# Kernel optimization log

Hardware: AMD Instinct MI355X
Metric: run time of the kernel (lower is better)

Reference implementation:

```python
import jax, jax.numpy as jnp
import numpy as np

HIDDEN = 384
HEADS = 8
DIM_HEAD = HIDDEN // HEADS  # 48
INNER = DIM_HEAD * HEADS
SCALE = DIM_HEAD ** -0.5


def setup_inputs() -> dict:
    key = jax.random.key(0)
    k1, k2, k3, k4 = jax.random.split(key, 4)
    B, C, D, H, W = 2, HIDDEN, 16, 16, 8
    x = jax.random.normal(k1, (B, C, D, H, W), dtype=jnp.float32)
    # nn.Linear weights (stored as [out, in] in torch; use [in, out] here)
    w_qkv = jax.random.normal(k2, (C, 3 * INNER), dtype=jnp.float32) * (C ** -0.5)
    w_out = jax.random.normal(k3, (INNER, C), dtype=jnp.float32) * (INNER ** -0.5)
    b_out = jax.random.normal(k4, (C,), dtype=jnp.float32) * 0.02
    return {"x": x, "w_qkv": w_qkv, "w_out": w_out, "b_out": b_out}


def reference(x, w_qkv, w_out, b_out):
    B, C, D, H, W = x.shape
    N = D * H * W
    tokens = x.reshape(B, C, N).transpose(0, 2, 1)          # [B, N, C]
    qkv = tokens @ w_qkv                                     # [B, N, 3*inner]
    qkv = qkv.reshape(B, N, 3, HEADS, DIM_HEAD).transpose(2, 0, 3, 1, 4)
    q, k, v = qkv[0], qkv[1], qkv[2]                         # [B, h, N, dh]
    q = jnp.clip(q, -5.0, 5.0)
    k = jnp.clip(k, -5.0, 5.0)
    logits = jnp.einsum('bhnd,bhmd->bhnm', q, k) * SCALE     # [B, h, N, N]
    logits = logits - jnp.max(logits, axis=-1, keepdims=True)
    attn = jax.nn.softmax(logits, axis=-1)
    out = jnp.einsum('bhnm,bhmd->bhnd', attn, v)             # [B, h, N, dh]
    out = out.transpose(0, 2, 1, 3).reshape(B, N, INNER)     # [B, N, inner]
    out = out @ w_out + b_out                                # [B, N, C]
    out = out.transpose(0, 2, 1).reshape(B, C, D, H, W)
    return x + out
```

## Files before the change

kernel.cpp:

```cpp
#include <hip/hip_runtime.h>

#define B_SZ 2
#define C_IN 384
#define N_TOK 2048
#define HEADS 8
#define DH 48
#define J3 1152
#define QSCALE_LOG2 0.20823509110768f
#define KSPLIT 4
#define KEYS_PER_SPLIT 512
#define DEFER_THR 11.0f

typedef __attribute__((ext_vector_type(8))) _Float16 f16x8;
typedef __attribute__((ext_vector_type(4))) _Float16 f16x4;
typedef __attribute__((ext_vector_type(4))) float f32x4;

__device__ __forceinline__ unsigned short f2h(float f) {
  _Float16 h = (_Float16)f;
  return __builtin_bit_cast(unsigned short, h);
}
__device__ __forceinline__ uint pk2(float a, float b) {
  return __builtin_bit_cast(uint, __builtin_amdgcn_cvt_pkrtz(a, b));
}
__device__ __forceinline__ float exp2g(float x) {
  return __builtin_amdgcn_exp2f(x);
}

__global__ __launch_bounds__(256) void qkv_mfma(
    const float* __restrict__ x, const float* __restrict__ wq,
    unsigned short* __restrict__ Qo, unsigned short* __restrict__ Ko,
    unsigned short* __restrict__ Vo) {
  __shared__ __align__(16) unsigned short Ts[128][72];
  __shared__ __align__(16) unsigned short Ws[64][72];
  __shared__ __align__(16) unsigned short Xt[64][132];
  __shared__ __align__(16) unsigned short Wt[64][68];
  const int tid = threadIdx.x;
  const int w = tid >> 6, lane = tid & 63;
  const int lc = lane & 15, lg = lane >> 4;
  const int m0 = blockIdx.x * 128;
  const int j0 = blockIdx.y * 64;
  const int b = m0 >> 11;
  const int n0 = m0 & 2047;

  f32x4 acc[2][4];
#pragma unroll
  for (int i = 0; i < 2; ++i)
#pragma unroll
    for (int j = 0; j < 4; ++j) acc[i][j] = (f32x4){0.f, 0.f, 0.f, 0.f};

  const float* xbase = x + (size_t)b * C_IN * N_TOK + n0;

  for (int kk = 0; kk < C_IN; kk += 64) {
#pragma unroll
    for (int i = 0; i < 8; ++i) {
      const int f = tid + 256 * i;
      const int c = f >> 5, m4 = (f & 31) * 4;
      const float4 v = *(const float4*)(xbase + (size_t)(kk + c) * N_TOK + m4);
      ushort4 h;
      h.x = f2h(v.x); h.y = f2h(v.y); h.z = f2h(v.z); h.w = f2h(v.w);
      *(ushort4*)&Xt[c][m4] = h;
    }
#pragma unroll
    for (int i = 0; i < 4; ++i) {
      const int f = tid + 256 * i;
      const int c = f >> 4, j4 = (f & 15) * 4;
      const float4 v = *(const float4*)(wq + (size_t)(kk + c) * J3 + j0 + j4);
      ushort4 h;
      h.x = f2h(v.x); h.y = f2h(v.y); h.z = f2h(v.z); h.w = f2h(v.w);
      *(ushort4*)&Wt[c][j4] = h;
    }
    __syncthreads();

    {
      const int m = tid >> 1, ks = (tid & 1) * 32;
      unsigned short tmp[32];
#pragma unroll
      for (int j2 = 0; j2 < 32; ++j2) tmp[j2] = Xt[ks + j2][m];
#pragma unroll
      for (int j2 = 0; j2 < 8; ++j2)
        *(ushort4*)&Ts[m][ks + 4 * j2] =
            make_ushort4(tmp[4 * j2], tmp[4 * j2 + 1], tmp[4 * j2 + 2], tmp[4 * j2 + 3]);
      const int jj = tid >> 2, ks2 = (tid & 3) * 16;
      unsigned short tw[16];
#pragma unroll
      for (int i2 = 0; i2 < 16; ++i2) tw[i2] = Wt[ks2 + i2][jj];
#pragma unroll
      for (int i2 = 0; i2 < 4; ++i2)
        *(ushort4*)&Ws[jj][ks2 + 4 * i2] =
            make_ushort4(tw[4 * i2], tw[4 * i2 + 1], tw[4 * i2 + 2], tw[4 * i2 + 3]);
    }
    __syncthreads();

    f16x8 a[2][2], bf[4][2];
#pragma unroll
    for (int mt = 0; mt < 2; ++mt)
#pragma unroll
      for (int kh = 0; kh < 2; ++kh)
        a[mt][kh] = *(const f16x8*)&Ts[32 * w + 16 * mt + lc][32 * kh + 8 * lg];
#pragma unroll
    for (int jt = 0; jt < 4; ++jt)
#pragma unroll
      for (int kh = 0; kh < 2; ++kh)
        bf[jt][kh] = *(const f16x8*)&Ws[16 * jt + lc][32 * kh + 8 * lg];
#pragma unroll
    for (int mt = 0; mt < 2; ++mt)
#pragma unroll
      for (int jt = 0; jt < 4; ++jt)
#pragma unroll
        for (int kh = 0; kh < 2; ++kh)
          acc[mt][jt] = __builtin_amdgcn_mfma_f32_16x16x32_f16(a[mt][kh], bf[jt][kh], acc[mt][jt], 0, 0, 0);
    __syncthreads();
  }

  if (j0 >= 768) {
    unsigned short* Tv = &Ts[0][0];
#pragma unroll
    for (int jt = 0; jt < 4; ++jt)
#pragma unroll
      for (int mt = 0; mt < 2; ++mt)
#pragma unroll
        for (int r = 0; r < 4; ++r)
          Tv[(16 * jt + lc) * 136 + (32 * w + 16 * mt + 4 * lg + r)] =
              f2h(acc[mt][jt][r]);
    __syncthreads();
#pragma unroll
    for (int i = 0; i < 4; ++i) {
      const int s = tid + i * 256;
      const int row = s >> 4;
      const int segoff = (s & 15) * 8;
      const int rr2 = j0 - 768 + row;
      const int head = rr2 / DH;
      const int d = rr2 - head * DH;
      const int bh = b * HEADS + head;
      *(uint4*)(Vo + ((size_t)bh * DH + d) * N_TOK + n0 + segoff) =
          *(const uint4*)&Tv[row * 136 + segoff];
    }
  } else {
#pragma unroll
    for (int jt = 0; jt < 4; ++jt) {
      const int jlo = j0 + 16 * jt;
      const int which = jlo / 384;
      const int rr = jlo - which * 384;
      const int head = rr / DH;
      const int dbase = rr - head * DH;
      const int d = dbase + lc;
      const int bh = b * HEADS + head;
#pragma unroll
      for (int mt = 0; mt < 2; ++mt)
#pragma unroll
        for (int r = 0; r < 4; ++r) {
          const int n = (m0 + 32 * w + 16 * mt + 4 * lg + r) & 2047;
          float val = fminf(fmaxf(acc[mt][jt][r], -5.f), 5.f);
          if (which == 0) {
            Qo[((size_t)bh * N_TOK + n) * DH + d] = f2h(val * QSCALE_LOG2);
          } else {
            Ko[((size_t)bh * N_TOK + n) * DH + d] = f2h(val);
          }
        }
    }
  }
}

__global__ __launch_bounds__(512) void attn_kernel(
    const unsigned short* __restrict__ Q, const unsigned short* __restrict__ K,
    const unsigned short* __restrict__ Vt, unsigned short* __restrict__ Opart,
    float2* __restrict__ ml) {
  const int qt = blockIdx.x, bh = blockIdx.y, ks = blockIdx.z;
  const int b = bh >> 3, h = bh & 7;
  const int n0 = qt * 128;
  const int tid = threadIdx.x;
  const int w = tid >> 6, lane = tid & 63;
  const int lc = lane & 15, lg = lane >> 4;

  __shared__ __align__(16) unsigned short Ks[2][64][56];
  __shared__ __align__(16) unsigned short Vs[2][48][68];

  const unsigned short* Qrow = Q + ((size_t)bh * N_TOK + n0 + 16 * w + lc) * DH;
  const f16x8 qf0 = *(const f16x8*)(Qrow + 8 * lg);
  f16x8 qf1 = {0, 0, 0, 0, 0, 0, 0, 0};
  {
    const f16x4 t = *(const f16x4*)(Qrow + 32 + 4 * lg);
    qf1[0] = t[0]; qf1[1] = t[1]; qf1[2] = t[2]; qf1[3] = t[3];
  }

  const unsigned short* Kg = K + (size_t)bh * N_TOK * DH + (size_t)ks * KEYS_PER_SPLIT * DH;
  const uint* Vg32 = (const uint*)(Vt + (size_t)bh * DH * N_TOK) + ks * (KEYS_PER_SPLIT / 2);

  uint kr[3], vr[3];
  auto issue = [&](int t0) {
    const uint* Ksrc = (const uint*)(Kg + (size_t)t0 * DH);
#pragma unroll
    for (int i = 0; i < 3; ++i) {
      const int dw = tid + i * 512;
      kr[i] = Ksrc[dw];
      vr[i] = Vg32[(size_t)(dw >> 5) * 1024 + (t0 >> 1) + (dw & 31)];
    }
  };
  auto commit = [&](int buf) {
#pragma unroll
    for (int i = 0; i < 3; ++i) {
      const int dw = tid + i * 512;
      const int key = dw / 24, c = dw - key * 24;
      *(uint*)&Ks[buf][key][2 * c] = kr[i];
      *(uint*)&Vs[buf][dw >> 5][2 * (dw & 31)] = vr[i];
    }
  };

  float m_run = -1e30f, l_run = 0.f;
  f32x4 oacc[3] = {{0,0,0,0},{0,0,0,0},{0,0,0,0}};

  issue(0);
  commit(0);

  for (int t = 0; t < KEYS_PER_SPLIT / 64; ++t) {
    const int cur = t & 1;
    if (t < KEYS_PER_SPLIT / 64 - 1) issue((t + 1) * 64);
    __syncthreads();

    f32x4 sac[4];
    __builtin_amdgcn_s_setprio(1);
#pragma unroll
    for (int it = 0; it < 4; ++it) {
      const int krow = 16 * it + lc;
      const f16x8 kf0 = *(const f16x8*)&Ks[cur][krow][8 * lg];
      f16x8 kf1 = {0, 0, 0, 0, 0, 0, 0, 0};
      const f16x4 tt = *(const f16x4*)&Ks[cur][krow][32 + 4 * lg];
      kf1[0] = tt[0]; kf1[1] = tt[1]; kf1[2] = tt[2]; kf1[3] = tt[3];
      const f32x4 z = {0.f, 0.f, 0.f, 0.f};
      f32x4 s = __builtin_amdgcn_mfma_f32_16x16x32_f16(kf0, qf0, z, 0, 0, 0);
      sac[it]  = __builtin_amdgcn_mfma_f32_16x16x32_f16(kf1, qf1, s, 0, 0, 0);
    }
    __builtin_amdgcn_s_setprio(0);

    float mt = -1e30f;
#pragma unroll
    for (int it = 0; it < 4; ++it)
#pragma unroll
      for (int r = 0; r < 4; ++r) mt = fmaxf(mt, sac[it][r]);
    mt = fmaxf(mt, __shfl_xor(mt, 16, 64));
    mt = fmaxf(mt, __shfl_xor(mt, 32, 64));

    if (!__all(mt - m_run <= DEFER_THR)) {
      const float mn = fmaxf(m_run, mt);
      const float rs = exp2g(m_run - mn);
      m_run = mn;
      l_run *= rs;
#pragma unroll
      for (int itd = 0; itd < 3; ++itd)
#pragma unroll
        for (int r = 0; r < 4; ++r) oacc[itd][r] *= rs;
    }

    float p[4][4];
    float ps = 0.f;
#pragma unroll
    for (int it = 0; it < 4; ++it)
#pragma unroll
      for (int r = 0; r < 4; ++r) {
        p[it][r] = exp2g(sac[it][r] - m_run);
        ps += p[it][r];
      }
    ps += __shfl_xor(ps, 16, 64);
    ps += __shfl_xor(ps, 32, 64);
    l_run += ps;

    f16x8 pt[2];
#pragma unroll
    for (int ks2 = 0; ks2 < 2; ++ks2) {
      union { f16x8 v; uint u[4]; } pu;
      pu.u[0] = pk2(p[2 * ks2][0], p[2 * ks2][1]);
      pu.u[1] = pk2(p[2 * ks2][2], p[2 * ks2][3]);
      pu.u[2] = pk2(p[2 * ks2 + 1][0], p[2 * ks2 + 1][1]);
      pu.u[3] = pk2(p[2 * ks2 + 1][2], p[2 * ks2 + 1][3]);
      pt[ks2] = pu.v;
    }

    __builtin_amdgcn_s_setprio(1);
#pragma unroll
    for (int itd = 0; itd < 3; ++itd) {
      const int drow = 16 * itd + lc;
#pragma unroll
      for (int ks2 = 0; ks2 < 2; ++ks2) {
        const f16x4 v0 = *(const f16x4*)&Vs[cur][drow][4 * lg + 32 * ks2];
        const f16x4 v1 = *(const f16x4*)&Vs[cur][drow][4 * lg + 32 * ks2 + 16];
        f16x8 vf;
        vf[0] = v0[0]; vf[1] = v0[1]; vf[2] = v0[2]; vf[3] = v0[3];
        vf[4] = v1[0]; vf[5] = v1[1]; vf[6] = v1[2]; vf[7] = v1[3];
        oacc[itd] = __builtin_amdgcn_mfma_f32_16x16x32_f16(vf, pt[ks2], oacc[itd], 0, 0, 0);
      }
    }
    __builtin_amdgcn_s_setprio(0);

    if (t < KEYS_PER_SPLIT / 64 - 1) commit(cur ^ 1);
  }

  if (lg == 0)
    ml[(size_t)(ks * 16 + bh) * N_TOK + n0 + 16 * w + lc] = make_float2(m_run, l_run);
  const float inv = 1.f / l_run;
  unsigned short* Ap = Opart +
      ((size_t)(ks * B_SZ + b) * N_TOK + n0 + 16 * w + lc) * 384 + h * DH;
#pragma unroll
  for (int itd = 0; itd < 3; ++itd) {
    uint2 pkv;
    pkv.x = pk2(oacc[itd][0] * inv, oacc[itd][1] * inv);
    pkv.y = pk2(oacc[itd][2] * inv, oacc[itd][3] * inv);
    *(uint2*)(Ap + 16 * itd + 4 * lg) = pkv;
  }
}

__global__ __launch_bounds__(256) void combine_kernel(
    const unsigned short* __restrict__ Opart, const float2* __restrict__ ml,
    unsigned short* __restrict__ AOh) {
  const int vid = blockIdx.x * 256 + threadIdx.x;
  const int c8 = vid % 48;
  const int n  = (vid / 48) & 2047;
  const int b  = vid / (48 * 2048);
  const int c0 = c8 * 8;
  const int h  = c0 / 48;
  const int bh = b * 8 + h;
  const size_t PS = (size_t)B_SZ * N_TOK * 384;
  float2 e0 = ml[(size_t)(0 * 16 + bh) * N_TOK + n];
  float2 e1 = ml[(size_t)(1 * 16 + bh) * N_TOK + n];
  float2 e2 = ml[(size_t)(2 * 16 + bh) * N_TOK + n];
  float2 e3 = ml[(size_t)(3 * 16 + bh) * N_TOK + n];
  const float M = fmaxf(fmaxf(e0.x, e1.x), fmaxf(e2.x, e3.x));
  const float g0 = exp2g(e0.x - M) * e0.y, g1 = exp2g(e1.x - M) * e1.y;
  const float g2 = exp2g(e2.x - M) * e2.y, g3 = exp2g(e3.x - M) * e3.y;
  const float inv = 1.f / (g0 + g1 + g2 + g3);
  const float s0 = g0 * inv, s1 = g1 * inv, s2 = g2 * inv, s3 = g3 * inv;
  const size_t o = ((size_t)b * N_TOK + n) * 384 + c0;
  union U8 { uint4 q; _Float16 e[8]; } u0, u1, u2, u3, r;
  u0.q = *(const uint4*)(Opart + 0 * PS + o);
  u1.q = *(const uint4*)(Opart + 1 * PS + o);
  u2.q = *(const uint4*)(Opart + 2 * PS + o);
  u3.q = *(const uint4*)(Opart + 3 * PS + o);
#pragma unroll
  for (int k = 0; k < 8; k += 2) {
    const float a = (float)u0.e[k] * s0 + (float)u1.e[k] * s1 +
                    (float)u2.e[k] * s2 + (float)u3.e[k] * s3;
    const float bb = (float)u0.e[k + 1] * s0 + (float)u1.e[k + 1] * s1 +
                     (float)u2.e[k + 1] * s2 + (float)u3.e[k + 1] * s3;
    *(uint*)&r.e[k] = pk2(a, bb);
  }
  *(uint4*)(AOh + o) = r.q;
}

__global__ __launch_bounds__(256) void proj_mfma(
    const unsigned short* __restrict__ AOh, const float* __restrict__ wo,
    const float* __restrict__ b_out, const float* __restrict__ x,
    float* __restrict__ out) {
  __shared__ __align__(16) unsigned short As[64][72];
  __shared__ __align__(16) unsigned short Bs[128][72];
  __shared__ __align__(16) unsigned short Wt2[64][68];
  const int tid = threadIdx.x;
  const int w = tid >> 6, lane = tid & 63;
  const int lc = lane & 15, lg = lane >> 4;
  const int c0 = blockIdx.x * 64;
  const int m0 = blockIdx.y * 128;
  const int b = m0 >> 11;

  f32x4 acc[4][2];
#pragma unroll
  for (int i = 0; i < 4; ++i)
#pragma unroll
    for (int j = 0; j < 2; ++j) acc[i][j] = (f32x4){0.f, 0.f, 0.f, 0.f};

  const int brow = tid & 127, bseg = tid >> 7;

  for (int kk = 0; kk < C_IN; kk += 64) {
#pragma unroll
    for (int i = 0; i < 4; ++i) {
      const int f = tid + 256 * i;
      const int c = f >> 4, c4 = (f & 15) * 4;
      const float4 v = *(const float4*)(wo + (size_t)(kk + c) * C_IN + c0 + c4);
      ushort4 h;
      h.x = f2h(v.x); h.y = f2h(v.y); h.z = f2h(v.z); h.w = f2h(v.w);
      *(ushort4*)&Wt2[c][c4] = h;
    }
    {
      const uint4* s2 = (const uint4*)(AOh + (size_t)(m0 + brow) * C_IN + kk + bseg * 32);
      uint4* d2 = (uint4*)&Bs[brow][bseg * 32];
      d2[0] = s2[0]; d2[1] = s2[1]; d2[2] = s2[2]; d2[3] = s2[3];
    }
    __syncthreads();

    {
      const int cc = tid >> 2, ks2 = (tid & 3) * 16;
      unsigned short tw[16];
#pragma unroll
      for (int i2 = 0; i2 < 16; ++i2) tw[i2] = Wt2[ks2 + i2][cc];
#pragma unroll
      for (int i2 = 0; i2 < 4; ++i2)
        *(ushort4*)&As[cc][ks2 + 4 * i2] =
            make_ushort4(tw[4 * i2], tw[4 * i2 + 1], tw[4 * i2 + 2], tw[4 * i2 + 3]);
    }
    __syncthreads();

    f16x8 a[4][2], bf[2][2];
#pragma unroll
    for (int ct = 0; ct < 4; ++ct)
#pragma unroll
      for (int kh = 0; kh < 2; ++kh)
        a[ct][kh] = *(const f16x8*)&As[16 * ct + lc][32 * kh + 8 * lg];
#pragma unroll
    for (int mt = 0; mt < 2; ++mt)
#pragma unroll
      for (int kh = 0; kh < 2; ++kh)
        bf[mt][kh] = *(const f16x8*)&Bs[32 * w + 16 * mt + lc][32 * kh + 8 * lg];
#pragma unroll
    for (int ct = 0; ct < 4; ++ct)
#pragma unroll
      for (int mt = 0; mt < 2; ++mt)
#pragma unroll
        for (int kh = 0; kh < 2; ++kh)
          acc[ct][mt] = __builtin_amdgcn_mfma_f32_16x16x32_f16(a[ct][kh], bf[mt][kh], acc[ct][mt], 0, 0, 0);
    __syncthreads();
  }

#pragma unroll
  for (int ct = 0; ct < 4; ++ct)
#pragma unroll
    for (int r = 0; r < 4; ++r) {
      const int c = c0 + 16 * ct + 4 * lg + r;
      const float bias = b_out[c];
#pragma unroll
      for (int mt = 0; mt < 2; ++mt) {
        const int n = (m0 + 32 * w + 16 * mt + lc) & 2047;
        const size_t off = ((size_t)b * C_IN + c) * N_TOK + n;
        out[off] = x[off] + bias + acc[ct][mt][r];
      }
    }
}

extern "C" void kernel_launch(void* const* d_in, const int* in_sizes, int n_in,
                              void* d_out, int out_size, void* d_ws, size_t ws_size,
                              hipStream_t stream) {
  const float* x     = (const float*)d_in[0];
  const float* w_qkv = (const float*)d_in[1];
  const float* w_out = (const float*)d_in[2];
  const float* b_out = (const float*)d_in[3];
  float* out = (float*)d_out;

  char* ws = (char*)d_ws;
  unsigned short* Qb    = (unsigned short*)(ws);
  unsigned short* Kb    = (unsigned short*)(ws + 3145728);
  unsigned short* Vb    = (unsigned short*)(ws + 6291456);
  unsigned short* Opart = (unsigned short*)(ws + 9437184);
  float2*         mlb   = (float2*)(ws + 22020096);
  unsigned short* AOh   = (unsigned short*)(ws + 23068672);

  qkv_mfma<<<dim3(32, 18), 256, 0, stream>>>(x, w_qkv, Qb, Kb, Vb);
  attn_kernel<<<dim3(16, 16, KSPLIT), 512, 0, stream>>>(Qb, Kb, Vb, Opart, mlb);
  combine_kernel<<<dim3(768), 256, 0, stream>>>(Opart, mlb, AOh);
  proj_mfma<<<dim3(6, 32), 256, 0, stream>>>(AOh, w_out, b_out, x, out);
}
```

Baseline: 71.59 us.

## Fuse split-K attention combine into output projection kernel

Removes the separate combine kernel. The projection kernel now merges the four split-K partial outputs for its 32-token tile directly into shared memory, using the per-split max/sum statistics, before running the MFMA projection. The projection tile changes from 64 channels by 128 tokens to 192 channels by 32 tokens, giving 256 blocks. This drops one launch and the round trip of the merged attention output through global memory. In exchange, each of the 128 token tiles repeats its combine work in both channel-half blocks, and the weight tile converted per step is larger.

After: 73.53 us. +2.7%, slower.

```diff
diff --git a/kernel.cpp b/kernel.cpp
--- a/kernel.cpp
+++ b/kernel.cpp
@@ -308,107 +308,108 @@
   }
 }
 
-__global__ __launch_bounds__(256) void combine_kernel(
+__global__ __launch_bounds__(256) void proj_mfma(
     const unsigned short* __restrict__ Opart, const float2* __restrict__ ml,
-    unsigned short* __restrict__ AOh) {
-  const int vid = blockIdx.x * 256 + threadIdx.x;
-  const int c8 = vid % 48;
-  const int n  = (vid / 48) & 2047;
-  const int b  = vid / (48 * 2048);
-  const int c0 = c8 * 8;
-  const int h  = c0 / 48;
-  const int bh = b * 8 + h;
-  const size_t PS = (size_t)B_SZ * N_TOK * 384;
-  float2 e0 = ml[(size_t)(0 * 16 + bh) * N_TOK + n];
-  float2 e1 = ml[(size_t)(1 * 16 + bh) * N_TOK + n];
-  float2 e2 = ml[(size_t)(2 * 16 + bh) * N_TOK + n];
-  float2 e3 = ml[(size_t)(3 * 16 + bh) * N_TOK + n];
-  const float M = fmaxf(fmaxf(e0.x, e1.x), fmaxf(e2.x, e3.x));
-  const float g0 = exp2g(e0.x - M) * e0.y, g1 = exp2g(e1.x - M) * e1.y;
-  const float g2 = exp2g(e2.x - M) * e2.y, g3 = exp2g(e3.x - M) * e3.y;
-  const float inv = 1.f / (g0 + g1 + g2 + g3);
-  const float s0 = g0 * inv, s1 = g1 * inv, s2 = g2 * inv, s3 = g3 * inv;
-  const size_t o = ((size_t)b * N_TOK + n) * 384 + c0;
-  union U8 { uint4 q; _Float16 e[8]; } u0, u1, u2, u3, r;
-  u0.q = *(const uint4*)(Opart + 0 * PS + o);
-  u1.q = *(const uint4*)(Opart + 1 * PS + o);
-  u2.q = *(const uint4*)(Opart + 2 * PS + o);
-  u3.q = *(const uint4*)(Opart + 3 * PS + o);
-#pragma unroll
-  for (int k = 0; k < 8; k += 2) {
-    const float a = (float)u0.e[k] * s0 + (float)u1.e[k] * s1 +
-                    (float)u2.e[k] * s2 + (float)u3.e[k] * s3;
-    const float bb = (float)u0.e[k + 1] * s0 + (float)u1.e[k + 1] * s1 +
-                     (float)u2.e[k + 1] * s2 + (float)u3.e[k + 1] * s3;
-    *(uint*)&r.e[k] = pk2(a, bb);
-  }
-  *(uint4*)(AOh + o) = r.q;
-}
-
-__global__ __launch_bounds__(256) void proj_mfma(
-    const unsigned short* __restrict__ AOh, const float* __restrict__ wo,
-    const float* __restrict__ b_out, const float* __restrict__ x,
-    float* __restrict__ out) {
-  __shared__ __align__(16) unsigned short As[64][72];
-  __shared__ __align__(16) unsigned short Bs[128][72];
-  __shared__ __align__(16) unsigned short Wt2[64][68];
+    const float* __restrict__ wo, const float* __restrict__ b_out,
+    const float* __restrict__ x, float* __restrict__ out) {
+  __shared__ __align__(16) unsigned short Bp[32][392];
+  __shared__ __align__(16) unsigned short As[192][72];
+  __shared__ __align__(16) unsigned short Wt2[64][200];
+  __shared__ float4 SW[32][8];
   const int tid = threadIdx.x;
   const int w = tid >> 6, lane = tid & 63;
   const int lc = lane & 15, lg = lane >> 4;
-  const int c0 = blockIdx.x * 64;
-  const int m0 = blockIdx.y * 128;
+  const int c0 = blockIdx.x * 192;
+  const int m0 = blockIdx.y * 32;
   const int b = m0 >> 11;
-
-  f32x4 acc[4][2];
-#pragma unroll
-  for (int i = 0; i < 4; ++i)
+  const int n0 = m0 & 2047;
+  const size_t PS = (size_t)B_SZ * N_TOK * 384;
+
+  {
+    const int mm = tid >> 3, hh = tid & 7;
+    const int n = n0 + mm;
+    const int bh = b * 8 + hh;
+    const float2 e0 = ml[(size_t)(0 * 16 + bh) * N_TOK + n];
+    const float2 e1 = ml[(size_t)(1 * 16 + bh) * N_TOK + n];
+    const float2 e2 = ml[(size_t)(2 * 16 + bh) * N_TOK + n];
+    const float2 e3 = ml[(size_t)(3 * 16 + bh) * N_TOK + n];
+    const float M = fmaxf(fmaxf(e0.x, e1.x), fmaxf(e2.x, e3.x));
+    const float g0 = exp2g(e0.x - M) * e0.y, g1 = exp2g(e1.x - M) * e1.y;
+    const float g2 = exp2g(e2.x - M) * e2.y, g3 = exp2g(e3.x - M) * e3.y;
+    const float ginv = 1.f / (g0 + g1 + g2 + g3);
+    SW[mm][hh] = make_float4(g0 * ginv, g1 * ginv, g2 * ginv, g3 * ginv);
+  }
+  __syncthreads();
+
+#pragma unroll
+  for (int i = 0; i < 6; ++i) {
+    const int idx = tid + 256 * i;
+    const int mm = idx / 48, seg = idx - mm * 48;
+    const int ce = seg * 8;
+    const float4 s4 = SW[mm][ce / 48];
+    const size_t o = ((size_t)b * N_TOK + n0 + mm) * 384 + ce;
+    union U8 { uint4 q; _Float16 e[8]; } u0, u1, u2, u3, r;
+    u0.q = *(const uint4*)(Opart + 0 * PS + o);
+    u1.q = *(const uint4*)(Opart + 1 * PS + o);
+    u2.q = *(const uint4*)(Opart + 2 * PS + o);
+    u3.q = *(const uint4*)(Opart + 3 * PS + o);
+#pragma unroll
+    for (int k = 0; k < 8; k += 2) {
+      const float a = (float)u0.e[k] * s4.x + (float)u1.e[k] * s4.y +
+                      (float)u2.e[k] * s4.z + (float)u3.e[k] * s4.w;
+      const float bb = (float)u0.e[k + 1] * s4.x + (float)u1.e[k + 1] * s4.y +
+                       (float)u2.e[k + 1] * s4.z + (float)u3.e[k + 1] * s4.w;
+      *(uint*)&r.e[k] = pk2(a, bb);
+    }
+    *(uint4*)&Bp[mm][ce] = r.q;
+  }
+  __syncthreads();
+
+  f32x4 acc[3][2];
+#pragma unroll
+  for (int i = 0; i < 3; ++i)
 #pragma unroll
     for (int j = 0; j < 2; ++j) acc[i][j] = (f32x4){0.f, 0.f, 0.f, 0.f};
 
-  const int brow = tid & 127, bseg = tid >> 7;
-
   for (int kk = 0; kk < C_IN; kk += 64) {
 #pragma unroll
-    for (int i = 0; i < 4; ++i) {
+    for (int i = 0; i < 12; ++i) {
       const int f = tid + 256 * i;
-      const int c = f >> 4, c4 = (f & 15) * 4;
-      const float4 v = *(const float4*)(wo + (size_t)(kk + c) * C_IN + c0 + c4);
+      const int row = f / 48, c4 = (f - row * 48) * 4;
+      const float4 v = *(const float4*)(wo + (size_t)(kk + row) * C_IN + c0 + c4);
       ushort4 h;
       h.x = f2h(v.x); h.y = f2h(v.y); h.z = f2h(v.z); h.w = f2h(v.w);
-      *(ushort4*)&Wt2[c][c4] = h;
-    }
-    {
-      const uint4* s2 = (const uint4*)(AOh + (size_t)(m0 + brow) * C_IN + kk + bseg * 32);
-      uint4* d2 = (uint4*)&Bs[brow][bseg * 32];
-      d2[0] = s2[0]; d2[1] = s2[1]; d2[2] = s2[2]; d2[3] = s2[3];
-    }
-    __syncthreads();
-
-    {
-      const int cc = tid >> 2, ks2 = (tid & 3) * 16;
+      *(ushort4*)&Wt2[row][c4] = h;
+    }
+    __syncthreads();
+
+    if (tid < 192) {
       unsigned short tw[16];
 #pragma unroll
-      for (int i2 = 0; i2 < 16; ++i2) tw[i2] = Wt2[ks2 + i2][cc];
-#pragma unroll
-      for (int i2 = 0; i2 < 4; ++i2)
-        *(ushort4*)&As[cc][ks2 + 4 * i2] =
-            make_ushort4(tw[4 * i2], tw[4 * i2 + 1], tw[4 * i2 + 2], tw[4 * i2 + 3]);
-    }
-    __syncthreads();
-
-    f16x8 a[4][2], bf[2][2];
-#pragma unroll
-    for (int ct = 0; ct < 4; ++ct)
+      for (int q = 0; q < 4; ++q) {
+#pragma unroll
+        for (int i2 = 0; i2 < 16; ++i2) tw[i2] = Wt2[16 * q + i2][tid];
+#pragma unroll
+        for (int i2 = 0; i2 < 4; ++i2)
+          *(ushort4*)&As[tid][16 * q + 4 * i2] =
+              make_ushort4(tw[4 * i2], tw[4 * i2 + 1], tw[4 * i2 + 2], tw[4 * i2 + 3]);
+      }
+    }
+    __syncthreads();
+
+    f16x8 a[3][2], bf[2][2];
+#pragma unroll
+    for (int ct = 0; ct < 3; ++ct)
 #pragma unroll
       for (int kh = 0; kh < 2; ++kh)
-        a[ct][kh] = *(const f16x8*)&As[16 * ct + lc][32 * kh + 8 * lg];
+        a[ct][kh] = *(const f16x8*)&As[48 * w + 16 * ct + lc][32 * kh + 8 * lg];
 #pragma unroll
     for (int mt = 0; mt < 2; ++mt)
 #pragma unroll
       for (int kh = 0; kh < 2; ++kh)
-        bf[mt][kh] = *(const f16x8*)&Bs[32 * w + 16 * mt + lc][32 * kh + 8 * lg];
-#pragma unroll
-    for (int ct = 0; ct < 4; ++ct)
+        bf[mt][kh] = *(const f16x8*)&Bp[16 * mt + lc][kk + 32 * kh + 8 * lg];
+#pragma unroll
+    for (int ct = 0; ct < 3; ++ct)
 #pragma unroll
       for (int mt = 0; mt < 2; ++mt)
 #pragma unroll
@@ -418,14 +419,14 @@
   }
 
 #pragma unroll
-  for (int ct = 0; ct < 4; ++ct)
+  for (int ct = 0; ct < 3; ++ct)
 #pragma unroll
     for (int r = 0; r < 4; ++r) {
-      const int c = c0 + 16 * ct + 4 * lg + r;
+      const int c = c0 + 48 * w + 16 * ct + 4 * lg + r;
       const float bias = b_out[c];
 #pragma unroll
       for (int mt = 0; mt < 2; ++mt) {
-        const int n = (m0 + 32 * w + 16 * mt + lc) & 2047;
+        const int n = n0 + 16 * mt + lc;
         const size_t off = ((size_t)b * C_IN + c) * N_TOK + n;
         out[off] = x[off] + bias + acc[ct][mt][r];
       }
@@ -447,10 +448,8 @@
   unsigned short* Vb    = (unsigned short*)(ws + 6291456);
   unsigned short* Opart = (unsigned short*)(ws + 9437184);
   float2*         mlb   = (float2*)(ws + 22020096);
-  unsigned short* AOh   = (unsigned short*)(ws + 23068672);
 
   qkv_mfma<<<dim3(32, 18), 256, 0, stream>>>(x, w_qkv, Qb, Kb, Vb);
   attn_kernel<<<dim3(16, 16, KSPLIT), 512, 0, stream>>>(Qb, Kb, Vb, Opart, mlb);
-  combine_kernel<<<dim3(768), 256, 0, stream>>>(Opart, mlb, AOh);
-  proj_mfma<<<dim3(6, 32), 256, 0, stream>>>(AOh, w_out, b_out, x, out);
-}
+  proj_mfma<<<dim3(2, 128), 256, 0, stream>>>(Opart, mlb, w_out, b_out, x, out);
+}
```
